# Kernel optimization log

Hardware: AMD Instinct MI355X
Metric: run time of the kernel (lower is better)

## Reference

```python
import jax, jax.numpy as jnp
import numpy as np

B, T, D, N, L, SCALE = 16, 4096, 256, 16, 4, 2
EPS_LN = 1e-5


def setup_inputs() -> dict:
    key = jax.random.key(0)
    ks = jax.random.split(key, 20)
    def w(k, shape, s):
        return jax.random.normal(k, shape, jnp.float32) * s
    inp = {"x": jax.random.normal(ks[0], (B, T, D), jnp.float32)}
    for i, pfx in enumerate(("fwd", "bwd")):
        b = 1 + i * 4
        inp[f"{pfx}_norm_w"] = jnp.ones((L, D), jnp.float32)
        inp[f"{pfx}_norm_b"] = jnp.zeros((L, D), jnp.float32)
        inp[f"{pfx}_dw"] = w(ks[b], (L, D, D), 1.0 / np.sqrt(D))
        inp[f"{pfx}_db"] = jnp.zeros((L, D), jnp.float32)
        inp[f"{pfx}_alog"] = w(ks[b + 1], (L, D, N), 0.02)
        inp[f"{pfx}_bparam"] = w(ks[b + 2], (L, D, N), 0.02)
        inp[f"{pfx}_ow"] = w(ks[b + 3], (L, D, D), 1.0 / np.sqrt(D))
        inp[f"{pfx}_ob"] = jnp.zeros((L, D), jnp.float32)
    inp["merge_w"] = w(ks[17], (2 * D, D), 1.0 / np.sqrt(2 * D))
    inp["merge_b"] = jnp.zeros((D,), jnp.float32)
    inp["scale"] = SCALE
    return inp


def _layernorm(x, g, b):
    m = x.mean(-1, keepdims=True)
    v = ((x - m) ** 2).mean(-1, keepdims=True)
    return (x - m) * jax.lax.rsqrt(v + EPS_LN) * g + b


def _ssm(x, dw, db, alog, bparam, ow, ob):
    # x: [B, Ts, D]; selective SSM recurrence over time (sequential scan).
    delta = jax.nn.softplus(x @ dw + db)          # [B, Ts, D]
    a_pos = jax.nn.softplus(alog) + 1e-4          # [D, N]
    s0 = jnp.zeros((x.shape[0], x.shape[2], a_pos.shape[1]), x.dtype)
    def step(state, td):
        x_t, d_t = td                             # each [B, D]
        state = jnp.exp(-d_t[:, :, None] * a_pos) * state + (d_t * x_t)[:, :, None] * bparam
        return state, state.sum(-1)               # y_t: [B, D]
    _, y = jax.lax.scan(step, s0, (jnp.swapaxes(x, 0, 1), jnp.swapaxes(delta, 0, 1)))
    return jnp.swapaxes(y, 0, 1) @ ow + ob


def _stack(x, nw, nb, dw, db, alog, bparam, ow, ob):
    # PreNorm -> SSM -> Residual, n_layers times (dropout=0 / eval)
    for l in range(nw.shape[0]):
        x = x + _ssm(_layernorm(x, nw[l], nb[l]), dw[l], db[l], alog[l], bparam[l], ow[l], ob[l])
    return x


def _upsample_linear(x, target_len):
    # matches F.interpolate(mode='linear', align_corners=False) on [B, Ts, D]
    in_len = x.shape[1]
    if in_len == target_len:
        return x
    pos = (jnp.arange(target_len, dtype=jnp.float32) + 0.5) * (in_len / target_len) - 0.5
    pos = jnp.clip(pos, 0.0, in_len - 1)
    lo = jnp.floor(pos).astype(jnp.int32)
    hi = jnp.minimum(lo + 1, in_len - 1)
    w = (pos - lo)[None, :, None]
    return x[:, lo, :] * (1.0 - w) + x[:, hi, :] * w


def reference(x, fwd_norm_w, fwd_norm_b, fwd_dw, fwd_db, fwd_alog, fwd_bparam, fwd_ow, fwd_ob,
              bwd_norm_w, bwd_norm_b, bwd_dw, bwd_db, bwd_alog, bwd_bparam, bwd_ow, bwd_ob,
              merge_w, merge_b, scale):
    target_len = x.shape[1]
    if scale != 1:
        b_, t_, d_ = x.shape
        # avg_pool1d(kernel=scale, stride=scale); T divisible by scale so ceil_mode is a no-op
        x_s = x.reshape(b_, t_ // scale, scale, d_).mean(2)
    else:
        x_s = x
    fwd = _stack(x_s, fwd_norm_w, fwd_norm_b, fwd_dw, fwd_db, fwd_alog, fwd_bparam, fwd_ow, fwd_ob)
    bwd = jnp.flip(_stack(jnp.flip(x_s, 1), bwd_norm_w, bwd_norm_b, bwd_dw, bwd_db, bwd_alog, bwd_bparam, bwd_ow, bwd_ob), 1)
    merged = jnp.concatenate([fwd, bwd], -1) @ merge_w + merge_b
    return _upsample_linear(merged, target_len)
```

## Files before the change

### kernel.cpp

```cpp
#include <hip/hip_runtime.h>


typedef __attribute__((ext_vector_type(8))) short short8;
typedef __attribute__((ext_vector_type(4))) float f32x4;

#define TS 2048
#define NSEQ_D 8192u
#define NCH 32
#define CLEN 64
#define LDSP 72

#if __has_builtin(__builtin_amdgcn_exp2f)
#define EXP2F(x) __builtin_amdgcn_exp2f(x)
#else
#define EXP2F(x) exp2f(x)
#endif
#if __has_builtin(__builtin_amdgcn_logf)
#define LOG2F(x) __builtin_amdgcn_logf(x)
#else
#define LOG2F(x) log2f(x)
#endif
#define LOG2E 1.44269504088896f
#define LN2 0.69314718055995f

__device__ __forceinline__ unsigned short f2bf(float f) {
  unsigned u = __float_as_uint(f);
  u = u + 0x7FFFu + ((u >> 16) & 1u);
  return (unsigned short)(u >> 16);
}
__device__ __forceinline__ float bf2f(unsigned short h) {
  return __uint_as_float(((unsigned)h) << 16);
}
__device__ __forceinline__ float softplus_fast(float x) {
  float e = EXP2F(-fabsf(x) * LOG2E);
  return fmaxf(x, 0.f) + LN2 * LOG2F(1.f + e);
}

__device__ __forceinline__ void gld16(const unsigned short* g, unsigned short* l) {
  __builtin_amdgcn_global_load_lds(
      (const __attribute__((address_space(1))) void*)g,
      (__attribute__((address_space(3))) void*)l, 16, 0, 0);
}

__global__ __launch_bounds__(256) void wconv_kernel(
    const float* __restrict__ fdw, const float* __restrict__ bdw,
    const float* __restrict__ fow, const float* __restrict__ bow,
    const float* __restrict__ mw,
    const float* __restrict__ falog, const float* __restrict__ balog,
    unsigned short* __restrict__ dwT, unsigned short* __restrict__ owT,
    unsigned short* __restrict__ mT, float* __restrict__ c2tab) {
  unsigned idx = blockIdx.x * 256u + threadIdx.x;
  if (idx < 524288u) {
    unsigned dir = idx >> 18, l = (idx >> 16) & 3u, n = (idx >> 8) & 255u, k = idx & 255u;
    const float* s = dir ? bdw : fdw;
    dwT[idx] = f2bf(s[((l << 8) + k) * 256u + n]);
  } else if (idx < 1048576u) {
    unsigned r = idx - 524288u;
    unsigned dir = r >> 18, l = (r >> 16) & 3u, n = (r >> 8) & 255u, k = r & 255u;
    const float* s = dir ? bow : fow;
    owT[r] = f2bf(s[((l << 8) + k) * 256u + n]);
  } else if (idx < 1179648u) {
    unsigned r = idx - 1048576u;
    unsigned n = r >> 9, k = r & 511u;
    mT[r] = f2bf(mw[(k << 8) + n]);
  } else {
    unsigned r = idx - 1179648u;
    unsigned dir = r >> 14;
    const float* s = dir ? balog : falog;
    c2tab[r] = -(softplus_fast(s[r & 16383u]) + 1e-4f) * LOG2E;
  }
}

__global__ __launch_bounds__(256) void ln0_kernel(
    const float* __restrict__ x, float* __restrict__ xw,
    unsigned short* __restrict__ xn,
    const float* __restrict__ fnw, const float* __restrict__ fnb,
    const float* __restrict__ bnw, const float* __restrict__ bnb) {
  unsigned row = (blockIdx.x << 2) + (threadIdx.x >> 6);
  unsigned lane = threadIdx.x & 63u;
  unsigned b = row >> 11, jj = row & 2047u;
  const float4* x4 = (const float4*)x;
  float4 v0 = x4[(((b << 12) + (jj << 1)) << 6) + lane];
  float4 v1 = x4[(((b << 12) + (jj << 1) + 1u) << 6) + lane];
  float4 p;
  p.x = 0.5f * (v0.x + v1.x); p.y = 0.5f * (v0.y + v1.y);
  p.z = 0.5f * (v0.z + v1.z); p.w = 0.5f * (v0.w + v1.w);
  float s = p.x + p.y + p.z + p.w;
  float q = p.x * p.x + p.y * p.y + p.z * p.z + p.w * p.w;
  for (int o = 32; o > 0; o >>= 1) { s += __shfl_xor(s, o); q += __shfl_xor(q, o); }
  float m = s * (1.f / 256.f);
  float rstd = rsqrtf(q * (1.f / 256.f) - m * m + 1e-5f);

  unsigned r0 = ((b << 11) + jj) << 6;
  unsigned r1 = ((((16u + b) << 11) + (2047u - jj)) << 6);
  ((float4*)xw)[r0 + lane] = p;
  ((float4*)xw)[r1 + lane] = p;

  unsigned dd = lane << 2;
  float zx = (p.x - m) * rstd, zy = (p.y - m) * rstd, zz = (p.z - m) * rstd, zw = (p.w - m) * rstd;
  ushort4 o0 = make_ushort4(
      f2bf(zx * fnw[dd] + fnb[dd]), f2bf(zy * fnw[dd + 1] + fnb[dd + 1]),
      f2bf(zz * fnw[dd + 2] + fnb[dd + 2]), f2bf(zw * fnw[dd + 3] + fnb[dd + 3]));
  ushort4 o1 = make_ushort4(
      f2bf(zx * bnw[dd] + bnb[dd]), f2bf(zy * bnw[dd + 1] + bnb[dd + 1]),
      f2bf(zz * bnw[dd + 2] + bnb[dd + 2]), f2bf(zw * bnw[dd + 3] + bnb[dd + 3]));
  ((ushort4*)xn)[r0 + lane] = o0;
  ((ushort4*)xn)[r1 + lane] = o1;
}

__global__ __launch_bounds__(256) void ln_kernel(
    const float* __restrict__ xw, unsigned short* __restrict__ xn,
    const float* __restrict__ fnw, const float* __restrict__ fnb,
    const float* __restrict__ bnw, const float* __restrict__ bnb, int l) {
  unsigned row = (blockIdx.x << 2) + (threadIdx.x >> 6);
  unsigned lane = threadIdx.x & 63u;
  unsigned dir = row >> 15;
  const float* g = (dir ? bnw : fnw) + (l << 8);
  const float* bb = (dir ? bnb : fnb) + (l << 8);
  float4 v = ((const float4*)xw)[(row << 6) + lane];
  float s = v.x + v.y + v.z + v.w;
  float q = v.x * v.x + v.y * v.y + v.z * v.z + v.w * v.w;
  for (int o = 32; o > 0; o >>= 1) { s += __shfl_xor(s, o); q += __shfl_xor(q, o); }
  float m = s * (1.f / 256.f);
  float var = q * (1.f / 256.f) - m * m;
  float r = rsqrtf(var + 1e-5f);
  unsigned dd = lane << 2;
  ushort4 o4 = make_ushort4(
      f2bf((v.x - m) * r * g[dd + 0] + bb[dd + 0]),
      f2bf((v.y - m) * r * g[dd + 1] + bb[dd + 1]),
      f2bf((v.z - m) * r * g[dd + 2] + bb[dd + 2]),
      f2bf((v.w - m) * r * g[dd + 3] + bb[dd + 3]));
  ((ushort4*)xn)[(row << 6) + lane] = o4;
}

template <int MODE>
__global__ __launch_bounds__(256) void gemm_layer_k(
    const unsigned short* __restrict__ Abf, const unsigned short* __restrict__ WT,
    const float* __restrict__ bias_f, const float* __restrict__ bias_b, int l,
    unsigned short* __restrict__ delta_out, float* __restrict__ xw) {
  __shared__ __align__(16) unsigned short As[2][64 * 64];
  __shared__ __align__(16) unsigned short Bs[2][256 * 64];
  const int tid = threadIdx.x;
  const int lane = tid & 63, wave = tid >> 6;
  const int wm = wave >> 1, wn = wave & 1;
  const int lrow = lane & 15, lhi = lane >> 4;
  const int r0 = blockIdx.x << 6;
  const int dir = r0 >> 15;
  const unsigned short* W = WT + (((dir << 2) + l) << 16);
  const float* bias = (dir ? bias_b : bias_f) + (l << 8);

  f32x4 acc[2][8] = {};

  auto issue = [&](int p, int k0) {
#pragma unroll
    for (int i = 0; i < 2; ++i) {
      int idx = (i << 8) + tid;
      int row = idx >> 3, scc = (idx & 7) ^ (row & 7);
      gld16(&Abf[(unsigned)(r0 + row) * 256u + (unsigned)(k0 + (scc << 3))],
            &As[p][idx << 3]);
    }
#pragma unroll
    for (int i = 0; i < 8; ++i) {
      int idx = (i << 8) + tid;
      int row = idx >> 3, scc = (idx & 7) ^ (row & 7);
      gld16(&W[(unsigned)row * 256u + (unsigned)(k0 + (scc << 3))],
            &Bs[p][idx << 3]);
    }
  };
  auto compute = [&](int p) {
#pragma unroll
    for (int kk = 0; kk < 2; ++kk) {
      short8 af[2], bfr[8];
#pragma unroll
      for (int m = 0; m < 2; ++m) {
        int row = (wm << 5) + (m << 4) + lrow;
        int slot = (row << 3) + (((kk << 2) + lhi) ^ (row & 7));
        af[m] = *(const short8*)&As[p][slot << 3];
      }
#pragma unroll
      for (int n = 0; n < 8; ++n) {
        int row = (wn << 7) + (n << 4) + lrow;
        int slot = (row << 3) + (((kk << 2) + lhi) ^ (row & 7));
        bfr[n] = *(const short8*)&Bs[p][slot << 3];
      }
#pragma unroll
      for (int m = 0; m < 2; ++m)
#pragma unroll
        for (int n = 0; n < 8; ++n)
          acc[m][n] = __builtin_amdgcn_mfma_f32_16x16x32_bf16(af[m], bfr[n], acc[m][n], 0, 0, 0);
    }
  };

  issue(0, 0);
  for (int it = 0; it < 4; ++it) {
    __syncthreads();
    if (it < 3) issue((it + 1) & 1, (it + 1) << 6);
    compute(it & 1);
  }

#pragma unroll
  for (int m = 0; m < 2; ++m) {
#pragma unroll
    for (int n = 0; n < 8; ++n) {
      const int col = (wn << 7) + (n << 4) + lrow;
      const float bv = bias[col];
#pragma unroll
      for (int j = 0; j < 4; ++j) {
        const unsigned grow = (unsigned)(r0 + (wm << 5) + (m << 4) + (lhi << 2) + j);
        float v = acc[m][n][j] + bv;
        if (MODE == 0) {
          delta_out[grow * 256u + (unsigned)col] = f2bf(softplus_fast(v));
        } else {
          xw[grow * 256u + (unsigned)col] += v;
        }
      }
    }
  }
}

__global__ __launch_bounds__(256) void scan_pass1(
    const unsigned short* __restrict__ delta, const unsigned short* __restrict__ xn,
    float4* __restrict__ SP, const float* __restrict__ c2tab, int l) {
  const unsigned gid = blockIdx.x * 256u + threadIdx.x;
  const unsigned seq = gid & (NSEQ_D - 1u);
  const unsigned c = gid >> 13;
  const int d = seq & 255;
  const unsigned seqrow = seq >> 8;
  const int dir = seq >> 12;
  const float4* c2p = (const float4*)&c2tab[(((unsigned)(dir << 2) + l) << 12) + ((unsigned)d << 4)];

  float c2[16];
#pragma unroll
  for (int q = 0; q < 4; ++q) {
    float4 cv = c2p[q];
    c2[q * 4 + 0] = cv.x; c2[q * 4 + 1] = cv.y; c2[q * 4 + 2] = cv.z; c2[q * 4 + 3] = cv.w;
  }

  const unsigned base = (seqrow << 19) + (((unsigned)c << 6) << 8) + (unsigned)d;
  float s[16];
#pragma unroll
  for (int n = 0; n < 16; ++n) s[n] = 0.f;
  float dsum = 0.f;

  for (int tt = 0; tt < CLEN; tt += 8) {
    const unsigned bb = base + ((unsigned)tt << 8);
    unsigned short dv[8], xv[8];
#pragma unroll
    for (int k = 0; k < 8; ++k) dv[k] = delta[bb + ((unsigned)k << 8)];
#pragma unroll
    for (int k = 0; k < 8; ++k) xv[k] = xn[bb + ((unsigned)k << 8)];
#pragma unroll
    for (int k = 0; k < 8; ++k) {
      float dt = bf2f(dv[k]);
      float u = dt * bf2f(xv[k]);
      dsum += dt;
#pragma unroll
      for (int n = 0; n < 16; ++n)
        s[n] = fmaf(EXP2F(c2[n] * dt), s[n], u);
    }
  }

  float4* o = &SP[(size_t)gid << 3];
#pragma unroll
  for (int q = 0; q < 4; ++q) {
    float4 v; v.x = s[q * 4]; v.y = s[q * 4 + 1]; v.z = s[q * 4 + 2]; v.w = s[q * 4 + 3];
    o[q] = v;
  }
#pragma unroll
  for (int q = 0; q < 4; ++q) {
    float4 v;
    v.x = EXP2F(c2[q * 4 + 0] * dsum); v.y = EXP2F(c2[q * 4 + 1] * dsum);
    v.z = EXP2F(c2[q * 4 + 2] * dsum); v.w = EXP2F(c2[q * 4 + 3] * dsum);
    o[4 + q] = v;
  }
}

__global__ __launch_bounds__(256) void scan_mid(float* __restrict__ SP) {
  const unsigned t = blockIdx.x * 256u + threadIdx.x;
  const unsigned seq = t >> 4;
  const unsigned n = t & 15u;
  float* base = SP + (size_t)seq * 32 + n;
  const size_t cstride = (size_t)NSEQ_D * 32;
  float sg = 0.f;
  for (int c = 0; c < NCH - 1; ++c) {
    float S = base[c * cstride];
    float P = base[c * cstride + 16];
    base[c * cstride] = sg;
    sg = fmaf(P, sg, S);
  }
  base[(NCH - 1) * cstride] = sg;
}

__global__ __launch_bounds__(256) void scan_pass2(
    const unsigned short* __restrict__ delta, const unsigned short* __restrict__ xn,
    unsigned short* __restrict__ y, const float4* __restrict__ SP,
    const float* __restrict__ c2tab,
    const float* __restrict__ bp_f, const float* __restrict__ bp_b, int l) {
  const unsigned gid = blockIdx.x * 256u + threadIdx.x;
  const unsigned seq = gid & (NSEQ_D - 1u);
  const unsigned c = gid >> 13;
  const int d = seq & 255;
  const unsigned seqrow = seq >> 8;
  const int dir = seq >> 12;
  const float4* c2p = (const float4*)&c2tab[(((unsigned)(dir << 2) + l) << 12) + ((unsigned)d << 4)];
  const float* bpp = (dir ? bp_b : bp_f) + (((l << 8) + d) << 4);

  float c2[16], bp[16];
#pragma unroll
  for (int q = 0; q < 4; ++q) {
    float4 cv = c2p[q];
    c2[q * 4 + 0] = cv.x; c2[q * 4 + 1] = cv.y; c2[q * 4 + 2] = cv.z; c2[q * 4 + 3] = cv.w;
    float4 bv = ((const float4*)bpp)[q];
    bp[q * 4 + 0] = bv.x; bp[q * 4 + 1] = bv.y; bp[q * 4 + 2] = bv.z; bp[q * 4 + 3] = bv.w;
  }

  float s[16];
  {
    const float4* sg = &SP[(size_t)gid << 3];
    float4 v0 = sg[0], v1 = sg[1], v2 = sg[2], v3 = sg[3];
    s[0] = v0.x; s[1] = v0.y; s[2] = v0.z; s[3] = v0.w;
    s[4] = v1.x; s[5] = v1.y; s[6] = v1.z; s[7] = v1.w;
    s[8] = v2.x; s[9] = v2.y; s[10] = v2.z; s[11] = v2.w;
    s[12] = v3.x; s[13] = v3.y; s[14] = v3.z; s[15] = v3.w;
  }

  const unsigned base = (seqrow << 19) + (((unsigned)c << 6) << 8) + (unsigned)d;

  for (int tt = 0; tt < CLEN; tt += 8) {
    const unsigned bb = base + ((unsigned)tt << 8);
    unsigned short dv[8], xv[8];
#pragma unroll
    for (int k = 0; k < 8; ++k) dv[k] = delta[bb + ((unsigned)k << 8)];
#pragma unroll
    for (int k = 0; k < 8; ++k) xv[k] = xn[bb + ((unsigned)k << 8)];
#pragma unroll
    for (int k = 0; k < 8; ++k) {
      float dt = bf2f(dv[k]);
      float u = dt * bf2f(xv[k]);
#pragma unroll
      for (int n = 0; n < 16; ++n)
        s[n] = fmaf(EXP2F(c2[n] * dt), s[n], u);
      float ya = bp[0] * s[0], yb = bp[1] * s[1], yc = bp[2] * s[2], yd = bp[3] * s[3];
      ya = fmaf(bp[4], s[4], ya);   yb = fmaf(bp[5], s[5], yb);
      yc = fmaf(bp[6], s[6], yc);   yd = fmaf(bp[7], s[7], yd);
      ya = fmaf(bp[8], s[8], ya);   yb = fmaf(bp[9], s[9], yb);
      yc = fmaf(bp[10], s[10], yc); yd = fmaf(bp[11], s[11], yd);
      ya = fmaf(bp[12], s[12], ya); yb = fmaf(bp[13], s[13], yb);
      yc = fmaf(bp[14], s[14], yc); yd = fmaf(bp[15], s[15], yd);
      float ys = (ya + yb) + (yc + yd);
      y[bb + ((unsigned)k << 8)] = f2bf(ys);
    }
  }
}

__global__ __launch_bounds__(256) void gemm_merge_k(
    const float* __restrict__ xw, const unsigned short* __restrict__ MT,
    const float* __restrict__ mb, float* __restrict__ merged) {
  __shared__ __align__(16) unsigned short As[64 * LDSP];
  __shared__ __align__(16) unsigned short Bs[256 * LDSP];
  const int tid = threadIdx.x;
  const int lane = tid & 63, wave = tid >> 6;
  const int wm = wave >> 1, wn = wave & 1;
  const int lrow = lane & 15, lhi = lane >> 4;
  const int r0 = blockIdx.x << 6;

  const int arow = tid >> 2, afo = (tid & 3) << 4;
  const int brow = tid;

  f32x4 acc[2][8] = {};

  for (int it = 0; it < 8; ++it) {
    const int k0 = it << 6;
    __syncthreads();
    {
      int gr = r0 + arow;
      int b = gr >> 11, t = gr & 2047;
      unsigned srcrow = (k0 < 256) ? (unsigned)(b * 2048 + t)
                                   : (unsigned)((16 + b) * 2048 + (2047 - t));
      const float4* ap = (const float4*)&xw[srcrow * 256u + (unsigned)((k0 & 255) + afo)];
      float4 rf[4];
#pragma unroll
      for (int i = 0; i < 4; ++i) rf[i] = ap[i];
      int4 rb[8];
      const unsigned bb = (unsigned)brow * 512u + (unsigned)k0;
#pragma unroll
      for (int i = 0; i < 8; ++i) rb[i] = *(const int4*)&MT[bb + (unsigned)(i << 3)];
#pragma unroll
      for (int i = 0; i < 2; ++i) {
        float4 f0 = rf[2 * i], f1 = rf[2 * i + 1];
        short8 pk;
        pk[0] = (short)f2bf(f0.x); pk[1] = (short)f2bf(f0.y);
        pk[2] = (short)f2bf(f0.z); pk[3] = (short)f2bf(f0.w);
        pk[4] = (short)f2bf(f1.x); pk[5] = (short)f2bf(f1.y);
        pk[6] = (short)f2bf(f1.z); pk[7] = (short)f2bf(f1.w);
        *(short8*)&As[arow * LDSP + afo + (i << 3)] = pk;
      }
#pragma unroll
      for (int i = 0; i < 8; ++i) *(int4*)&Bs[brow * LDSP + (i << 3)] = rb[i];
    }
    __syncthreads();
#pragma unroll
    for (int kk = 0; kk < 2; ++kk) {
      short8 af[2], bfr[8];
#pragma unroll
      for (int m = 0; m < 2; ++m)
        af[m] = *(const short8*)&As[((wm << 5) + (m << 4) + lrow) * LDSP + (kk << 5) + (lhi << 3)];
#pragma unroll
      for (int n = 0; n < 8; ++n)
        bfr[n] = *(const short8*)&Bs[((wn << 7) + (n << 4) + lrow) * LDSP + (kk << 5) + (lhi << 3)];
#pragma unroll
      for (int m = 0; m < 2; ++m)
#pragma unroll
        for (int n = 0; n < 8; ++n)
          acc[m][n] = __builtin_amdgcn_mfma_f32_16x16x32_bf16(af[m], bfr[n], acc[m][n], 0, 0, 0);
    }
  }

#pragma unroll
  for (int m = 0; m < 2; ++m) {
#pragma unroll
    for (int n = 0; n < 8; ++n) {
      const int col = (wn << 7) + (n << 4) + lrow;
      const float bv = mb[col];
#pragma unroll
      for (int j = 0; j < 4; ++j) {
        const unsigned grow = (unsigned)(r0 + (wm << 5) + (m << 4) + (lhi << 2) + j);
        merged[grow * 256u + (unsigned)col] = acc[m][n][j] + bv;
      }
    }
  }
}

__global__ __launch_bounds__(256) void up_kernel(const float4* __restrict__ m4,
                                                 float4* __restrict__ out4) {
  unsigned idx = blockIdx.x * 256u + threadIdx.x;
  unsigned d4 = idx & 63u;
  unsigned t = (idx >> 6) & 4095u;
  unsigned b = idx >> 18;
  unsigned j = t >> 1;
  unsigned lo, hi; float wlo, whi;
  if (t & 1u) { lo = j; hi = (j < 2047u) ? j + 1u : 2047u; wlo = 0.75f; whi = 0.25f; }
  else { lo = j ? j - 1u : 0u; hi = j; wlo = 0.25f; whi = 0.75f; }
  float4 a = m4[((b << 11) + lo) * 64u + d4];
  float4 c = m4[((b << 11) + hi) * 64u + d4];
  float4 o;
  o.x = wlo * a.x + whi * c.x; o.y = wlo * a.y + whi * c.y;
  o.z = wlo * a.z + whi * c.z; o.w = wlo * a.w + whi * c.w;
  out4[((b << 12) + t) * 64u + d4] = o;
}

extern "C" void kernel_launch(void* const* d_in, const int* in_sizes, int n_in,
                              void* d_out, int out_size, void* d_ws, size_t ws_size,
                              hipStream_t stream) {
  const float* x    = (const float*)d_in[0];
  const float* fnw  = (const float*)d_in[1];
  const float* fnb  = (const float*)d_in[2];
  const float* fdw  = (const float*)d_in[3];
  const float* fdb  = (const float*)d_in[4];
  const float* falog = (const float*)d_in[5];
  const float* fbp  = (const float*)d_in[6];
  const float* fow  = (const float*)d_in[7];
  const float* fob  = (const float*)d_in[8];
  const float* bnw  = (const float*)d_in[9];
  const float* bnb  = (const float*)d_in[10];
  const float* bdw  = (const float*)d_in[11];
  const float* bdb  = (const float*)d_in[12];
  const float* balog = (const float*)d_in[13];
  const float* bbp  = (const float*)d_in[14];
  const float* bow  = (const float*)d_in[15];
  const float* bob  = (const float*)d_in[16];
  const float* mw   = (const float*)d_in[17];
  const float* mb   = (const float*)d_in[18];

  char* ws = (char*)d_ws;
  const size_t SZ = 33554432;
  unsigned short* xn_bf  = (unsigned short*)(ws);
  unsigned short* delta  = (unsigned short*)(ws + SZ);
  unsigned short* y_bf   = (unsigned short*)(ws + 2 * SZ);
  float4* SP             = (float4*)(ws + 3 * SZ);
  unsigned short* dwT    = (unsigned short*)(ws + 4 * SZ);
  unsigned short* owT    = dwT + 524288;
  unsigned short* mergeT = owT + 524288;
  float* c2tab           = (float*)(mergeT + 131072);
  float* merged          = (float*)delta;
  float* xw              = (float*)d_out;

  wconv_kernel<<<4736, 256, 0, stream>>>(fdw, bdw, fow, bow, mw, falog, balog,
                                         dwT, owT, mergeT, c2tab);
  ln0_kernel<<<8192, 256, 0, stream>>>(x, xw, xn_bf, fnw, fnb, bnw, bnb);

  for (int l = 0; l < 4; ++l) {
    if (l > 0)
      ln_kernel<<<16384, 256, 0, stream>>>(xw, xn_bf, fnw, fnb, bnw, bnb, l);
    gemm_layer_k<0><<<1024, 256, 0, stream>>>(xn_bf, dwT, fdb, bdb, l, delta, nullptr);
    scan_pass1<<<32 * (NCH - 1), 256, 0, stream>>>(delta, xn_bf, SP, c2tab, l);
    scan_mid<<<512, 256, 0, stream>>>((float*)SP);
    scan_pass2<<<32 * NCH, 256, 0, stream>>>(delta, xn_bf, y_bf, SP, c2tab, fbp, bbp, l);
    gemm_layer_k<1><<<1024, 256, 0, stream>>>(y_bf, owT, fob, bob, l, nullptr, xw);
  }

  gemm_merge_k<<<512, 256, 0, stream>>>(xw, mergeT, mb, merged);
  up_kernel<<<16384, 256, 0, stream>>>((const float4*)merged, (float4*)d_out);
}
```

Before: 730.5 us.

## Store residual stream in bf16 and pipeline merge GEMM with async swizzled loads

The residual stream xw is now kept in bf16 instead of fp32, which halves its traffic in the layernorm, the residual-add epilogue and the merge GEMM. The merge GEMM is rewritten to match the layer GEMM: double-buffered LDS filled by gld16 direct loads with an XOR swizzle, replacing the synchronous fp32-load-then-convert path. This removes per-tile conversion work and overlaps loads with MFMA compute. In exchange, accumulating residuals in bf16 across four layers loses precision and raises numerical error.

```diff
diff --git a/kernel.cpp b/kernel.cpp
--- a/kernel.cpp
+++ b/kernel.cpp
@@ -8,7 +8,6 @@
 #define NSEQ_D 8192u
 #define NCH 32
 #define CLEN 64
-#define LDSP 72
 
 #if __has_builtin(__builtin_amdgcn_exp2f)
 #define EXP2F(x) __builtin_amdgcn_exp2f(x)
@@ -72,7 +71,7 @@
 }
 
 __global__ __launch_bounds__(256) void ln0_kernel(
-    const float* __restrict__ x, float* __restrict__ xw,
+    const float* __restrict__ x, unsigned short* __restrict__ xwb,
     unsigned short* __restrict__ xn,
     const float* __restrict__ fnw, const float* __restrict__ fnb,
     const float* __restrict__ bnw, const float* __restrict__ bnb) {
@@ -93,8 +92,9 @@
 
   unsigned r0 = ((b << 11) + jj) << 6;
   unsigned r1 = ((((16u + b) << 11) + (2047u - jj)) << 6);
-  ((float4*)xw)[r0 + lane] = p;
-  ((float4*)xw)[r1 + lane] = p;
+  ushort4 pw = make_ushort4(f2bf(p.x), f2bf(p.y), f2bf(p.z), f2bf(p.w));
+  ((ushort4*)xwb)[r0 + lane] = pw;
+  ((ushort4*)xwb)[r1 + lane] = pw;
 
   unsigned dd = lane << 2;
   float zx = (p.x - m) * rstd, zy = (p.y - m) * rstd, zz = (p.z - m) * rstd, zw = (p.w - m) * rstd;
@@ -109,7 +109,7 @@
 }
 
 __global__ __launch_bounds__(256) void ln_kernel(
-    const float* __restrict__ xw, unsigned short* __restrict__ xn,
+    const unsigned short* __restrict__ xwb, unsigned short* __restrict__ xn,
     const float* __restrict__ fnw, const float* __restrict__ fnb,
     const float* __restrict__ bnw, const float* __restrict__ bnb, int l) {
   unsigned row = (blockIdx.x << 2) + (threadIdx.x >> 6);
@@ -117,19 +117,20 @@
   unsigned dir = row >> 15;
   const float* g = (dir ? bnw : fnw) + (l << 8);
   const float* bb = (dir ? bnb : fnb) + (l << 8);
-  float4 v = ((const float4*)xw)[(row << 6) + lane];
-  float s = v.x + v.y + v.z + v.w;
-  float q = v.x * v.x + v.y * v.y + v.z * v.z + v.w * v.w;
+  ushort4 w4 = ((const ushort4*)xwb)[(row << 6) + lane];
+  float vx = bf2f(w4.x), vy = bf2f(w4.y), vz = bf2f(w4.z), vw = bf2f(w4.w);
+  float s = vx + vy + vz + vw;
+  float q = vx * vx + vy * vy + vz * vz + vw * vw;
   for (int o = 32; o > 0; o >>= 1) { s += __shfl_xor(s, o); q += __shfl_xor(q, o); }
   float m = s * (1.f / 256.f);
   float var = q * (1.f / 256.f) - m * m;
   float r = rsqrtf(var + 1e-5f);
   unsigned dd = lane << 2;
   ushort4 o4 = make_ushort4(
-      f2bf((v.x - m) * r * g[dd + 0] + bb[dd + 0]),
-      f2bf((v.y - m) * r * g[dd + 1] + bb[dd + 1]),
-      f2bf((v.z - m) * r * g[dd + 2] + bb[dd + 2]),
-      f2bf((v.w - m) * r * g[dd + 3] + bb[dd + 3]));
+      f2bf((vx - m) * r * g[dd + 0] + bb[dd + 0]),
+      f2bf((vy - m) * r * g[dd + 1] + bb[dd + 1]),
+      f2bf((vz - m) * r * g[dd + 2] + bb[dd + 2]),
+      f2bf((vw - m) * r * g[dd + 3] + bb[dd + 3]));
   ((ushort4*)xn)[(row << 6) + lane] = o4;
 }
 
@@ -137,7 +138,7 @@
 __global__ __launch_bounds__(256) void gemm_layer_k(
     const unsigned short* __restrict__ Abf, const unsigned short* __restrict__ WT,
     const float* __restrict__ bias_f, const float* __restrict__ bias_b, int l,
-    unsigned short* __restrict__ delta_out, float* __restrict__ xw) {
+    unsigned short* __restrict__ delta_out, unsigned short* __restrict__ xwb) {
   __shared__ __align__(16) unsigned short As[2][64 * 64];
   __shared__ __align__(16) unsigned short Bs[2][256 * 64];
   const int tid = threadIdx.x;
@@ -207,11 +208,12 @@
 #pragma unroll
       for (int j = 0; j < 4; ++j) {
         const unsigned grow = (unsigned)(r0 + (wm << 5) + (m << 4) + (lhi << 2) + j);
+        const unsigned gi = grow * 256u + (unsigned)col;
         float v = acc[m][n][j] + bv;
         if (MODE == 0) {
-          delta_out[grow * 256u + (unsigned)col] = f2bf(softplus_fast(v));
+          delta_out[gi] = f2bf(softplus_fast(v));
         } else {
-          xw[grow * 256u + (unsigned)col] += v;
+          xwb[gi] = f2bf(bf2f(xwb[gi]) + v);
         }
       }
     }
@@ -354,66 +356,67 @@
 }
 
 __global__ __launch_bounds__(256) void gemm_merge_k(
-    const float* __restrict__ xw, const unsigned short* __restrict__ MT,
+    const unsigned short* __restrict__ xwb, const unsigned short* __restrict__ MT,
     const float* __restrict__ mb, float* __restrict__ merged) {
-  __shared__ __align__(16) unsigned short As[64 * LDSP];
-  __shared__ __align__(16) unsigned short Bs[256 * LDSP];
+  __shared__ __align__(16) unsigned short As[2][64 * 64];
+  __shared__ __align__(16) unsigned short Bs[2][256 * 64];
   const int tid = threadIdx.x;
   const int lane = tid & 63, wave = tid >> 6;
   const int wm = wave >> 1, wn = wave & 1;
   const int lrow = lane & 15, lhi = lane >> 4;
   const int r0 = blockIdx.x << 6;
 
-  const int arow = tid >> 2, afo = (tid & 3) << 4;
-  const int brow = tid;
-
   f32x4 acc[2][8] = {};
 
-  for (int it = 0; it < 8; ++it) {
-    const int k0 = it << 6;
-    __syncthreads();
-    {
-      int gr = r0 + arow;
+  auto issue = [&](int p, int k0) {
+#pragma unroll
+    for (int i = 0; i < 2; ++i) {
+      int idx = (i << 8) + tid;
+      int row = idx >> 3, scc = (idx & 7) ^ (row & 7);
+      int gr = r0 + row;
       int b = gr >> 11, t = gr & 2047;
       unsigned srcrow = (k0 < 256) ? (unsigned)(b * 2048 + t)
                                    : (unsigned)((16 + b) * 2048 + (2047 - t));
-      const float4* ap = (const float4*)&xw[srcrow * 256u + (unsigned)((k0 & 255) + afo)];
-      float4 rf[4];
-#pragma unroll
-      for (int i = 0; i < 4; ++i) rf[i] = ap[i];
-      int4 rb[8];
-      const unsigned bb = (unsigned)brow * 512u + (unsigned)k0;
-#pragma unroll
-      for (int i = 0; i < 8; ++i) rb[i] = *(const int4*)&MT[bb + (unsigned)(i << 3)];
-#pragma unroll
-      for (int i = 0; i < 2; ++i) {
-        float4 f0 = rf[2 * i], f1 = rf[2 * i + 1];
-        short8 pk;
-        pk[0] = (short)f2bf(f0.x); pk[1] = (short)f2bf(f0.y);
-        pk[2] = (short)f2bf(f0.z); pk[3] = (short)f2bf(f0.w);
-        pk[4] = (short)f2bf(f1.x); pk[5] = (short)f2bf(f1.y);
-        pk[6] = (short)f2bf(f1.z); pk[7] = (short)f2bf(f1.w);
-        *(short8*)&As[arow * LDSP + afo + (i << 3)] = pk;
-      }
-#pragma unroll
-      for (int i = 0; i < 8; ++i) *(int4*)&Bs[brow * LDSP + (i << 3)] = rb[i];
-    }
-    __syncthreads();
+      gld16(&xwb[srcrow * 256u + (unsigned)((k0 & 255) + (scc << 3))],
+            &As[p][idx << 3]);
+    }
+#pragma unroll
+    for (int i = 0; i < 8; ++i) {
+      int idx = (i << 8) + tid;
+      int row = idx >> 3, scc = (idx & 7) ^ (row & 7);
+      gld16(&MT[(unsigned)row * 512u + (unsigned)(k0 + (scc << 3))],
+            &Bs[p][idx << 3]);
+    }
+  };
+  auto compute = [&](int p) {
 #pragma unroll
     for (int kk = 0; kk < 2; ++kk) {
       short8 af[2], bfr[8];
 #pragma unroll
-      for (int m = 0; m < 2; ++m)
-        af[m] = *(const short8*)&As[((wm << 5) + (m << 4) + lrow) * LDSP + (kk << 5) + (lhi << 3)];
-#pragma unroll
-      for (int n = 0; n < 8; ++n)
-        bfr[n] = *(const short8*)&Bs[((wn << 7) + (n << 4) + lrow) * LDSP + (kk << 5) + (lhi << 3)];
+      for (int m = 0; m < 2; ++m) {
+        int row = (wm << 5) + (m << 4) + lrow;
+        int slot = (row << 3) + (((kk << 2) + lhi) ^ (row & 7));
+        af[m] = *(const short8*)&As[p][slot << 3];
+      }
+#pragma unroll
+      for (int n = 0; n < 8; ++n) {
+        int row = (wn << 7) + (n << 4) + lrow;
+        int slot = (row << 3) + (((kk << 2) + lhi) ^ (row & 7));
+        bfr[n] = *(const short8*)&Bs[p][slot << 3];
+      }
 #pragma unroll
       for (int m = 0; m < 2; ++m)
 #pragma unroll
         for (int n = 0; n < 8; ++n)
           acc[m][n] = __builtin_amdgcn_mfma_f32_16x16x32_bf16(af[m], bfr[n], acc[m][n], 0, 0, 0);
     }
+  };
+
+  issue(0, 0);
+  for (int it = 0; it < 8; ++it) {
+    __syncthreads();
+    if (it < 7) issue((it + 1) & 1, (it + 1) << 6);
+    compute(it & 1);
   }
 
 #pragma unroll
@@ -483,22 +486,22 @@
   unsigned short* mergeT = owT + 524288;
   float* c2tab           = (float*)(mergeT + 131072);
   float* merged          = (float*)delta;
-  float* xw              = (float*)d_out;
+  unsigned short* xwb    = (unsigned short*)d_out;
 
   wconv_kernel<<<4736, 256, 0, stream>>>(fdw, bdw, fow, bow, mw, falog, balog,
                                          dwT, owT, mergeT, c2tab);
-  ln0_kernel<<<8192, 256, 0, stream>>>(x, xw, xn_bf, fnw, fnb, bnw, bnb);
+  ln0_kernel<<<8192, 256, 0, stream>>>(x, xwb, xn_bf, fnw, fnb, bnw, bnb);
 
   for (int l = 0; l < 4; ++l) {
     if (l > 0)
-      ln_kernel<<<16384, 256, 0, stream>>>(xw, xn_bf, fnw, fnb, bnw, bnb, l);
+      ln_kernel<<<16384, 256, 0, stream>>>(xwb, xn_bf, fnw, fnb, bnw, bnb, l);
     gemm_layer_k<0><<<1024, 256, 0, stream>>>(xn_bf, dwT, fdb, bdb, l, delta, nullptr);
     scan_pass1<<<32 * (NCH - 1), 256, 0, stream>>>(delta, xn_bf, SP, c2tab, l);
     scan_mid<<<512, 256, 0, stream>>>((float*)SP);
     scan_pass2<<<32 * NCH, 256, 0, stream>>>(delta, xn_bf, y_bf, SP, c2tab, fbp, bbp, l);
-    gemm_layer_k<1><<<1024, 256, 0, stream>>>(y_bf, owT, fob, bob, l, nullptr, xw);
-  }
-
-  gemm_merge_k<<<512, 256, 0, stream>>>(xw, mergeT, mb, merged);
+    gemm_layer_k<1><<<1024, 256, 0, stream>>>(y_bf, owT, fob, bob, l, nullptr, xwb);
+  }
+
+  gemm_merge_k<<<512, 256, 0, stream>>>(xwb, mergeT, mb, merged);
   up_kernel<<<16384, 256, 0, stream>>>((const float4*)merged, (float4*)d_out);
 }
```

Measured after the change: 654.2 us, median of 2. 10.4% less time.
